# Optimization experiments

Hardware: AMD Instinct MI355X
Metric: run time of the kernel (lower is better)

## Reference

```python
import jax, jax.numpy as jnp
import numpy as np

V, E, H = 50000, 300, 512
L, N, K = 6, 8192, 4


def setup_inputs() -> dict:
    key = jax.random.key(0)
    ks = jax.random.split(key, 12)
    vocab_ix = jax.random.randint(ks[0], (L, N), 0, V)
    child_idx = jax.random.randint(ks[1], (L, N, K), 0, N)
    token_mask = jnp.ones((L, N), dtype=jnp.float32)
    child_mask = (jax.random.uniform(ks[2], (L, N, K)) < 0.75).astype(jnp.float32)
    s = 0.02
    embed = jax.random.normal(ks[3], (V, E), dtype=jnp.float32)
    W_iou = jax.random.normal(ks[4], (E, 3 * H), dtype=jnp.float32) * s
    U_iou = jax.random.normal(ks[5], (H, 3 * H), dtype=jnp.float32) * s
    b_iou = jnp.zeros((3 * H,), dtype=jnp.float32)
    W_f = jax.random.normal(ks[6], (E, H), dtype=jnp.float32) * s
    U_f = jax.random.normal(ks[7], (H, H), dtype=jnp.float32) * s
    b_f = jnp.zeros((H,), dtype=jnp.float32)
    return {"vocab_ix": vocab_ix, "child_idx": child_idx, "token_mask": token_mask,
            "child_mask": child_mask, "embed": embed, "W_iou": W_iou, "U_iou": U_iou,
            "b_iou": b_iou, "W_f": W_f, "U_f": U_f, "b_f": b_f}


def _tree_lstm(vocab_ix, child_idx, token_mask, child_mask,
               embed, W_iou, U_iou, b_iou, W_f, U_f, b_f):
    # bottom-up over levels; level L-1 = leaves (no children -> zero prev states)
    h = jnp.zeros((N, H), dtype=embed.dtype)
    c = jnp.zeros((N, H), dtype=embed.dtype)
    for l in reversed(range(L)):
        # word2vec: embedding lookup; zero vector for non-token nodes
        x = embed[vocab_ix[l]] * token_mask[l][:, None]            # [N, E]
        xWf = x @ W_f                                              # [N, H]
        if l == L - 1:
            h_tilde = jnp.zeros((N, H), dtype=x.dtype)
            fc = jnp.zeros((N, H), dtype=x.dtype)
        else:
            m = child_mask[l][:, :, None]                          # [N, K, 1]
            h_ch = h[child_idx[l]] * m                             # [N, K, H]
            c_ch = c[child_idx[l]] * m                             # [N, K, H]
            h_tilde = h_ch.sum(axis=1)                             # child-sum
            # per-child forget gates (padded slots: c_ch is 0 -> no contribution)
            f = jax.nn.sigmoid(xWf[:, None, :] + jnp.einsum('nkh,hj->nkj', h_ch, U_f) + b_f)
            fc = (f * c_ch).sum(axis=1)
        iou = x @ W_iou + h_tilde @ U_iou + b_iou                  # [N, 3H]
        i, o, u = jnp.split(iou, 3, axis=-1)
        c = jax.nn.sigmoid(i) * jnp.tanh(u) + fc
        h = jax.nn.sigmoid(o) * jnp.tanh(c)
    return h  # outputs[0][1]: hidden states of root level


def reference(vocab_ix, child_idx, token_mask, child_mask,
              embed, W_iou, U_iou, b_iou, W_f, U_f, b_f):
    return _tree_lstm(vocab_ix, child_idx, token_mask, child_mask,
                      embed, W_iou, U_iou, b_iou, W_f, U_f, b_f)
```

## Files before the change

kernel.cpp:

```cpp
#include <hip/hip_runtime.h>
#include <cmath>

#define VSZ  50000
#define EDIM 300
#define EPAD 320
#define HDIM 512
#define LVLS 6
#define NN   8192
#define KCH  4

#define BM 128
#define BN 128
#define BK 32

typedef __attribute__((ext_vector_type(8))) short bf16x8;
typedef __attribute__((ext_vector_type(8))) unsigned short us8;
typedef __attribute__((ext_vector_type(4))) float f32x4;

__device__ __forceinline__ float sigf(float x) { return 1.0f / (1.0f + expf(-x)); }

__device__ __forceinline__ unsigned short f2bf(float f) {
    unsigned u = __float_as_uint(f);
    u += 0x7FFF + ((u >> 16) & 1);
    return (unsigned short)(u >> 16);
}
__device__ __forceinline__ float bf2f(unsigned short h) {
    return __uint_as_float(((unsigned)h) << 16);
}

__device__ __forceinline__ unsigned cvt_pk_bf16(float lo, float hi) {
    unsigned r;
    asm("v_cvt_pk_bf16_f32 %0, %1, %2" : "=v"(r) : "v"(lo), "v"(hi));
    return r;
}

__global__ __launch_bounds__(256) void gconv_k(
    const float* __restrict__ embed, const int* __restrict__ vix,
    const float* __restrict__ tmask, unsigned short* __restrict__ out)
{
    int t  = blockIdx.x * 256 + threadIdx.x;
    int r  = t / (EPAD / 8);
    int j8 = (t - r * (EPAD / 8)) * 8;
    float m = tmask[r];
    int   v = vix[r];
    const float* src = embed + (size_t)v * EDIM + j8;
    us8 o;
    if (j8 + 8 <= EDIM) {
        float4 a = *(const float4*)(src);
        float4 b = *(const float4*)(src + 4);
        const float xs[8] = {a.x, a.y, a.z, a.w, b.x, b.y, b.z, b.w};
#pragma unroll
        for (int j = 0; j < 8; ++j) o[j] = f2bf(xs[j] * m);
    } else {
#pragma unroll
        for (int j = 0; j < 8; ++j) {
            float x = (j8 + j < EDIM) ? src[j] * m : 0.0f;
            o[j] = f2bf(x);
        }
    }
    *(us8*)(out + (size_t)r * EPAD + j8) = o;
}

__global__ __launch_bounds__(256) void wconv_k(
    const float* __restrict__ in, unsigned short* __restrict__ out,
    int Kreal, int Ksp, int Nd)
{
    int t = blockIdx.x * 256 + threadIdx.x;
    int k = t % Ksp;
    int n = t / Ksp;
    out[t] = (k < Kreal) ? f2bf(in[(size_t)k * Nd + n]) : (unsigned short)0;
}

#define GLL(src, dst)                                                        \
    __builtin_amdgcn_global_load_lds(                                        \
        (const __attribute__((address_space(1))) unsigned int*)(src), (dst), 16, 0, 0)

template <int EPI, int NCHUNK>
__global__ __launch_bounds__(256) void mgemm_k(
    const unsigned short* __restrict__ Ab,
    const unsigned short* __restrict__ Bt,
    const float* __restrict__ b_iou, const float* __restrict__ b_f,
    unsigned short* __restrict__ C, int ldc, int Ks)
{
    __shared__ __align__(16) unsigned short smem[6 * BM * BK];

    const int tid  = threadIdx.x;
    const int wave = tid >> 6;
    const int lane = tid & 63;
    const int quad = lane >> 4;
    const int mcol = lane & 15;
    const int wm   = (wave >> 1) * 64;
    const int wn   = (wave & 1) * 64;
    const int band = wave >> 1;

    const int GX   = gridDim.x;
    const int P    = blockIdx.x + GX * blockIdx.y;
    const int g    = P & 7;
    const int s    = P >> 3;
    const int mper = gridDim.y >> 3;
    const int sdiv = s / GX;
    const int my_mt = g * mper + sdiv;
    const int my_ng = s - sdiv * GX;
    const int tile_m = my_mt * BM;

    const int r0  = tid >> 2;
    const int kg0 = (tid & 3) ^ ((r0 >> 1) & 3);
    const int cc1 = tid + 256;
    const int r1  = cc1 >> 2;
    const int kg1 = (cc1 & 3) ^ ((r1 >> 1) & 3);

    const unsigned short* asrc0 = Ab + (size_t)(tile_m + r0) * Ks + kg0 * 8;
    const unsigned short* asrc1 = Ab + (size_t)(tile_m + r1) * Ks + kg1 * 8;

    typedef __attribute__((address_space(3))) unsigned int lds_u32;

    float* eb = reinterpret_cast<float*>(smem);
    const int erl = tid >> 3;
    const int ecg = tid & 7;

#define STAGE3(kk, bo)                                                       \
    {                                                                        \
        GLL(asrc0 + (kk), (lds_u32*)(smem + (bo) + wave * 512));             \
        GLL(asrc1 + (kk), (lds_u32*)(smem + (bo) + 2048 + wave * 512));      \
        GLL(bsrc0 + (kk), (lds_u32*)(smem + (bo) + 4096 + wave * 512));      \
        GLL(bsrc1 + (kk), (lds_u32*)(smem + (bo) + 6144 + wave * 512));      \
    }
#define WAITV4  asm volatile("s_waitcnt vmcnt(4)" ::: "memory")
#define WAITV0  asm volatile("s_waitcnt vmcnt(0)" ::: "memory")
#define BAR     __builtin_amdgcn_s_barrier()

#define COMPUTE(bo)                                                         \
    {                                                                       \
        const unsigned short* AS = smem + (bo);                             \
        const unsigned short* BS = smem + (bo) + 4096;                      \
        bf16x8 afr[4], bfr[4];                                              \
        _Pragma("unroll")                                                   \
        for (int mt = 0; mt < 4; ++mt) {                                    \
            int rw = wm + mt * 16 + mcol;                                   \
            int p  = rw * 4 + (quad ^ ((rw >> 1) & 3));                     \
            afr[mt] = *(const bf16x8*)(AS + p * 8);                         \
        }                                                                   \
        _Pragma("unroll")                                                   \
        for (int nt = 0; nt < 4; ++nt) {                                    \
            int rw = wn + nt * 16 + mcol;                                   \
            int p  = rw * 4 + (quad ^ ((rw >> 1) & 3));                     \
            bfr[nt] = *(const bf16x8*)(BS + p * 8);                         \
        }                                                                   \
        _Pragma("unroll")                                                   \
        for (int mt = 0; mt < 4; ++mt)                                      \
            _Pragma("unroll")                                               \
            for (int nt = 0; nt < 4; ++nt)                                  \
                acc[mt][nt] = __builtin_amdgcn_mfma_f32_16x16x32_bf16(      \
                    afr[mt], bfr[nt], acc[mt][nt], 0, 0, 0);                \
    }

    for (int nc = 0; nc < NCHUNK; ++nc) {
        const int tile_n = (my_ng * NCHUNK + nc) * BN;
        const unsigned short* bsrc0 = Bt + (size_t)(tile_n + r0) * Ks + kg0 * 8;
        const unsigned short* bsrc1 = Bt + (size_t)(tile_n + r1) * Ks + kg1 * 8;

        f32x4 acc[4][4] = {};
        const int nsteps = Ks / BK;

        int bo0 = 0, bo1 = 8192, bo2 = 16384;

        STAGE3(0, bo0);
        STAGE3(BK, bo1);
        WAITV4;
        BAR;

        for (int st = 0; st < nsteps; ++st) {
            const bool pf = (st + 2 < nsteps);
            if (pf) STAGE3((st + 2) * BK, bo2);
            COMPUTE(bo0);
            if (pf) { WAITV4; } else { WAITV0; }
            BAR;
            int t0 = bo0; bo0 = bo1; bo1 = bo2; bo2 = t0;
        }

#pragma unroll
        for (int mt = 0; mt < 4; ++mt) {
            const int rbase = band * 16 + quad * 4;
#pragma unroll
            for (int nt = 0; nt < 4; ++nt) {
                const int cb = wn + nt * 16 + mcol;
                const int gq = cb >> 2;
                const int cl = cb & 3;
#pragma unroll
                for (int rr = 0; rr < 4; ++rr) {
                    const int r = rbase + rr;
                    eb[r * 128 + ((gq ^ (r & 7)) << 2) + cl] = acc[mt][nt][rr];
                }
            }
            __syncthreads();

            const int grow = tile_m + (erl >> 4) * 64 + mt * 16 + (erl & 15);
            const int gcol = tile_n + ecg * 16;
            float v[16];
#pragma unroll
            for (int sxt = 0; sxt < 4; ++sxt) {
                const int pg = (ecg * 4 + sxt) ^ (erl & 7);
                f32x4 q = *(const f32x4*)&eb[erl * 128 + pg * 4];
                v[sxt * 4 + 0] = q[0]; v[sxt * 4 + 1] = q[1];
                v[sxt * 4 + 2] = q[2]; v[sxt * 4 + 3] = q[3];
            }
            if (EPI == 1) {
                const float* bp = (gcol < 3 * HDIM) ? (b_iou + gcol)
                                                    : (b_f + gcol - 3 * HDIM);
                float4 b0 = *(const float4*)(bp);
                float4 b1 = *(const float4*)(bp + 4);
                float4 b2 = *(const float4*)(bp + 8);
                float4 b3 = *(const float4*)(bp + 12);
                const float bb[16] = {b0.x, b0.y, b0.z, b0.w, b1.x, b1.y, b1.z, b1.w,
                                      b2.x, b2.y, b2.z, b2.w, b3.x, b3.y, b3.z, b3.w};
#pragma unroll
                for (int j = 0; j < 16; ++j) v[j] += bb[j];
            }
            unsigned pw[8];
#pragma unroll
            for (int j = 0; j < 8; ++j) pw[j] = cvt_pk_bf16(v[2 * j], v[2 * j + 1]);
            unsigned short* cp = C + (size_t)grow * ldc + gcol;
            *(uint4*)(cp)     = make_uint4(pw[0], pw[1], pw[2], pw[3]);
            *(uint4*)(cp + 8) = make_uint4(pw[4], pw[5], pw[6], pw[7]);
            __syncthreads();
        }
    }
#undef STAGE3
#undef WAITV4
#undef WAITV0
#undef BAR
#undef COMPUTE
}

template <bool LAST>
__global__ __launch_bounds__(256) void gatefc_k(
    const unsigned short* __restrict__ iouxW, const unsigned short* __restrict__ Z,
    const int* __restrict__ cidx, const float* __restrict__ cmask,
    const float* __restrict__ c_prev,
    float* __restrict__ c_new, unsigned short* __restrict__ hb_new,
    float* __restrict__ h_out)
{
    int t  = blockIdx.x * 256 + threadIdx.x;
    int n  = t >> 6;
    int j8 = (t & 63) << 3;
    const unsigned short* xr = iouxW + (size_t)n * 4 * HDIM + j8;
    us8 xi = *(const us8*)xr;
    us8 xo = *(const us8*)(xr + HDIM);
    us8 xu = *(const us8*)(xr + 2 * HDIM);
    us8 xf = *(const us8*)(xr + 3 * HDIM);
    float ia[8], oa[8], ua[8], xw[8], fc[8];
#pragma unroll
    for (int j = 0; j < 8; ++j) {
        ia[j] = bf2f(xi[j]); oa[j] = bf2f(xo[j]);
        ua[j] = bf2f(xu[j]); xw[j] = bf2f(xf[j]);
        fc[j] = 0.0f;
    }
    int4   ci = *(const int4*)&cidx[n * KCH];
    float4 cm = *(const float4*)&cmask[n * KCH];
    const int   cia[4] = {ci.x, ci.y, ci.z, ci.w};
    const float cma[4] = {cm.x, cm.y, cm.z, cm.w};
#pragma unroll
    for (int k = 0; k < KCH; ++k) {
        const float m = cma[k];
        const unsigned short* zr = Z + (size_t)cia[k] * 4 * HDIM + j8;
        us8 zi = *(const us8*)zr;
        us8 zo = *(const us8*)(zr + HDIM);
        us8 zu = *(const us8*)(zr + 2 * HDIM);
        us8 zf = *(const us8*)(zr + 3 * HDIM);
        const float* cpr = c_prev + (size_t)cia[k] * HDIM + j8;
        float4 ca = *(const float4*)cpr;
        float4 cb = *(const float4*)(cpr + 4);
        const float cp[8] = {ca.x, ca.y, ca.z, ca.w, cb.x, cb.y, cb.z, cb.w};
#pragma unroll
        for (int j = 0; j < 8; ++j) {
            ia[j] += m * bf2f(zi[j]);
            oa[j] += m * bf2f(zo[j]);
            ua[j] += m * bf2f(zu[j]);
            fc[j] += sigf(xw[j] + m * bf2f(zf[j])) * m * cp[j];
        }
    }
    float cv[8], hv[8];
#pragma unroll
    for (int j = 0; j < 8; ++j) {
        cv[j] = sigf(ia[j]) * tanhf(ua[j]) + fc[j];
        hv[j] = sigf(oa[j]) * tanhf(cv[j]);
    }
    if (LAST) {
        float4 h0 = make_float4(hv[0], hv[1], hv[2], hv[3]);
        float4 h1 = make_float4(hv[4], hv[5], hv[6], hv[7]);
        *(float4*)(h_out + (size_t)n * HDIM + j8)     = h0;
        *(float4*)(h_out + (size_t)n * HDIM + j8 + 4) = h1;
    } else {
        float4 c0v = make_float4(cv[0], cv[1], cv[2], cv[3]);
        float4 c1v = make_float4(cv[4], cv[5], cv[6], cv[7]);
        *(float4*)(c_new + (size_t)n * HDIM + j8)     = c0v;
        *(float4*)(c_new + (size_t)n * HDIM + j8 + 4) = c1v;
        us8 hb;
#pragma unroll
        for (int j = 0; j < 8; ++j) hb[j] = f2bf(hv[j]);
        *(us8*)(hb_new + (size_t)n * HDIM + j8) = hb;
    }
}

__global__ __launch_bounds__(256) void gateleaf_k(
    const unsigned short* __restrict__ iouxW,
    float* __restrict__ c_new, unsigned short* __restrict__ hb_new)
{
    int t  = blockIdx.x * 256 + threadIdx.x;
    int n  = t >> 6;
    int j8 = (t & 63) << 3;
    const unsigned short* xr = iouxW + (size_t)n * 4 * HDIM + j8;
    us8 xi = *(const us8*)xr;
    us8 xo = *(const us8*)(xr + HDIM);
    us8 xu = *(const us8*)(xr + 2 * HDIM);
    float cv[8], hv[8];
#pragma unroll
    for (int j = 0; j < 8; ++j) {
        cv[j] = sigf(bf2f(xi[j])) * tanhf(bf2f(xu[j]));
        hv[j] = sigf(bf2f(xo[j])) * tanhf(cv[j]);
    }
    float4 c0v = make_float4(cv[0], cv[1], cv[2], cv[3]);
    float4 c1v = make_float4(cv[4], cv[5], cv[6], cv[7]);
    *(float4*)(c_new + (size_t)n * HDIM + j8)     = c0v;
    *(float4*)(c_new + (size_t)n * HDIM + j8 + 4) = c1v;
    us8 hb;
#pragma unroll
    for (int j = 0; j < 8; ++j) hb[j] = f2bf(hv[j]);
    *(us8*)(hb_new + (size_t)n * HDIM + j8) = hb;
}

extern "C" void kernel_launch(void* const* d_in, const int* in_sizes, int n_in,
                              void* d_out, int out_size, void* d_ws, size_t ws_size,
                              hipStream_t stream)
{
    const int*   vocab_ix   = (const int*)d_in[0];
    const int*   child_idx  = (const int*)d_in[1];
    const float* token_mask = (const float*)d_in[2];
    const float* child_mask = (const float*)d_in[3];
    const float* embed      = (const float*)d_in[4];
    const float* W_iou      = (const float*)d_in[5];
    const float* U_iou      = (const float*)d_in[6];
    const float* b_iou      = (const float*)d_in[7];
    const float* W_f        = (const float*)d_in[8];
    const float* U_f        = (const float*)d_in[9];
    const float* b_f        = (const float*)d_in[10];
    float* out = (float*)d_out;

    float* ws = (float*)d_ws;
    float* c0 = ws;
    float* c1 = c0 + (size_t)NN * HDIM;
    unsigned short* usb   = (unsigned short*)(c1 + (size_t)NN * HDIM);
    unsigned short* hb0   = usb;
    unsigned short* hb1   = hb0 + (size_t)NN * HDIM;
    unsigned short* iouxW = hb1 + (size_t)NN * HDIM;
    unsigned short* Z     = iouxW + (size_t)3 * NN * 4 * HDIM;
    unsigned short* AbatA = Z + (size_t)NN * 4 * HDIM;
    unsigned short* AbatB = AbatA + (size_t)3 * NN * EPAD;
    unsigned short* WtALL = AbatB + (size_t)3 * NN * EPAD;
    unsigned short* UtALL = WtALL + (size_t)4 * HDIM * EPAD;

    dim3 blk(256);

    const int grows = 3 * NN * (EPAD / 8) / 256;
    gconv_k<<<dim3(grows), blk, 0, stream>>>(embed, vocab_ix + (size_t)3 * NN,
                                             token_mask + (size_t)3 * NN, AbatA);
    gconv_k<<<dim3(grows), blk, 0, stream>>>(embed, vocab_ix, token_mask, AbatB);
    wconv_k<<<dim3(3 * HDIM * EPAD / 256), blk, 0, stream>>>(W_iou, WtALL, EDIM, EPAD, 3 * HDIM);
    wconv_k<<<dim3(HDIM * EPAD / 256),     blk, 0, stream>>>(W_f, WtALL + (size_t)3 * HDIM * EPAD, EDIM, EPAD, HDIM);
    wconv_k<<<dim3(3 * HDIM * HDIM / 256), blk, 0, stream>>>(U_iou, UtALL, HDIM, HDIM, 3 * HDIM);
    wconv_k<<<dim3(HDIM * HDIM / 256),     blk, 0, stream>>>(U_f, UtALL + (size_t)3 * HDIM * HDIM, HDIM, HDIM, HDIM);

    unsigned short* bbuf[2] = { hb0, hb1 };
    float*          cbuf[2] = { c0,  c1  };

    const int ew_blocks = NN * HDIM / 8 / 256;

    mgemm_k<1, 2><<<dim3(8, 3 * NN / BM), blk, 0, stream>>>(
        AbatA, WtALL, b_iou, b_f, iouxW, 4 * HDIM, EPAD);

    for (int l = LVLS - 1; l >= 0; --l) {
        const int p = (LVLS - 1 - l);
        unsigned short* hb_new  = bbuf[p & 1];
        float*          c_new   = cbuf[p & 1];
        unsigned short* hb_prev = bbuf[(p & 1) ^ 1];
        float*          c_prev  = cbuf[(p & 1) ^ 1];
        const int*   cix = child_idx  + (size_t)l * NN * KCH;
        const float* cm  = child_mask + (size_t)l * NN * KCH;
        const unsigned short* ix_l =
            iouxW + (size_t)((l >= 3) ? (l - 3) : l) * NN * 4 * HDIM;

        if (l == LVLS - 1) {
            gateleaf_k<<<dim3(ew_blocks), blk, 0, stream>>>(ix_l, c_new, hb_new);
        } else {
            mgemm_k<0, 2><<<dim3(8, NN / BM), blk, 0, stream>>>(
                hb_prev, UtALL, nullptr, nullptr, Z, 4 * HDIM, HDIM);

            if (l == 0) {
                gatefc_k<true><<<dim3(ew_blocks), blk, 0, stream>>>(
                    ix_l, Z, cix, cm, c_prev, nullptr, nullptr, out);
            } else {
                gatefc_k<false><<<dim3(ew_blocks), blk, 0, stream>>>(
                    ix_l, Z, cix, cm, c_prev, c_new, hb_new, nullptr);
            }
        }

        if (l == 3) {
            mgemm_k<1, 2><<<dim3(8, 3 * NN / BM), blk, 0, stream>>>(
                AbatB, WtALL, b_iou, b_f, iouxW, 4 * HDIM, EPAD);
        }
    }
}
```

Measured before the change: 598.5 us.

## Swap MFMA operands for direct bf16 epilogue stores; split recurrent GEMM grid

```diff
diff --git a/kernel.cpp b/kernel.cpp
--- a/kernel.cpp
+++ b/kernel.cpp
@@ -91,7 +91,6 @@
     const int mcol = lane & 15;
     const int wm   = (wave >> 1) * 64;
     const int wn   = (wave & 1) * 64;
-    const int band = wave >> 1;
 
     const int GX   = gridDim.x;
     const int P    = blockIdx.x + GX * blockIdx.y;
@@ -113,10 +112,6 @@
     const unsigned short* asrc1 = Ab + (size_t)(tile_m + r1) * Ks + kg1 * 8;
 
     typedef __attribute__((address_space(3))) unsigned int lds_u32;
-
-    float* eb = reinterpret_cast<float*>(smem);
-    const int erl = tid >> 3;
-    const int ecg = tid & 7;
 
 #define STAGE3(kk, bo)                                                       \
     {                                                                        \
@@ -151,7 +146,7 @@
             _Pragma("unroll")                                               \
             for (int nt = 0; nt < 4; ++nt)                                  \
                 acc[mt][nt] = __builtin_amdgcn_mfma_f32_16x16x32_bf16(      \
-                    afr[mt], bfr[nt], acc[mt][nt], 0, 0, 0);                \
+                    bfr[nt], afr[mt], acc[mt][nt], 0, 0, 0);                \
     }
 
     for (int nc = 0; nc < NCHUNK; ++nc) {
@@ -180,50 +175,25 @@
 
 #pragma unroll
         for (int mt = 0; mt < 4; ++mt) {
-            const int rbase = band * 16 + quad * 4;
+            const int grow = tile_m + wm + mt * 16 + mcol;
+            unsigned short* crow = C + (size_t)grow * ldc;
 #pragma unroll
             for (int nt = 0; nt < 4; ++nt) {
-                const int cb = wn + nt * 16 + mcol;
-                const int gq = cb >> 2;
-                const int cl = cb & 3;
-#pragma unroll
-                for (int rr = 0; rr < 4; ++rr) {
-                    const int r = rbase + rr;
-                    eb[r * 128 + ((gq ^ (r & 7)) << 2) + cl] = acc[mt][nt][rr];
+                const int col0 = tile_n + wn + nt * 16 + quad * 4;
+                float v0 = acc[mt][nt][0], v1 = acc[mt][nt][1];
+                float v2 = acc[mt][nt][2], v3 = acc[mt][nt][3];
+                if (EPI == 1) {
+                    const float* bp = (col0 < 3 * HDIM) ? (b_iou + col0)
+                                                        : (b_f + col0 - 3 * HDIM);
+                    float4 bb = *(const float4*)bp;
+                    v0 += bb.x; v1 += bb.y; v2 += bb.z; v3 += bb.w;
                 }
+                unsigned p0 = cvt_pk_bf16(v0, v1);
+                unsigned p1 = cvt_pk_bf16(v2, v3);
+                *(uint2*)(crow + col0) = make_uint2(p0, p1);
             }
-            __syncthreads();
-
-            const int grow = tile_m + (erl >> 4) * 64 + mt * 16 + (erl & 15);
-            const int gcol = tile_n + ecg * 16;
-            float v[16];
-#pragma unroll
-            for (int sxt = 0; sxt < 4; ++sxt) {
-                const int pg = (ecg * 4 + sxt) ^ (erl & 7);
-                f32x4 q = *(const f32x4*)&eb[erl * 128 + pg * 4];
-                v[sxt * 4 + 0] = q[0]; v[sxt * 4 + 1] = q[1];
-                v[sxt * 4 + 2] = q[2]; v[sxt * 4 + 3] = q[3];
-            }
-            if (EPI == 1) {
-                const float* bp = (gcol < 3 * HDIM) ? (b_iou + gcol)
-                                                    : (b_f + gcol - 3 * HDIM);
-                float4 b0 = *(const float4*)(bp);
-                float4 b1 = *(const float4*)(bp + 4);
-                float4 b2 = *(const float4*)(bp + 8);
-                float4 b3 = *(const float4*)(bp + 12);
-                const float bb[16] = {b0.x, b0.y, b0.z, b0.w, b1.x, b1.y, b1.z, b1.w,
-                                      b2.x, b2.y, b2.z, b2.w, b3.x, b3.y, b3.z, b3.w};
-#pragma unroll
-                for (int j = 0; j < 16; ++j) v[j] += bb[j];
-            }
-            unsigned pw[8];
-#pragma unroll
-            for (int j = 0; j < 8; ++j) pw[j] = cvt_pk_bf16(v[2 * j], v[2 * j + 1]);
-            unsigned short* cp = C + (size_t)grow * ldc + gcol;
-            *(uint4*)(cp)     = make_uint4(pw[0], pw[1], pw[2], pw[3]);
-            *(uint4*)(cp + 8) = make_uint4(pw[4], pw[5], pw[6], pw[7]);
-            __syncthreads();
-        }
+        }
+        if (nc + 1 < NCHUNK) BAR;
     }
 #undef STAGE3
 #undef WAITV4
@@ -392,7 +362,7 @@
         if (l == LVLS - 1) {
             gateleaf_k<<<dim3(ew_blocks), blk, 0, stream>>>(ix_l, c_new, hb_new);
         } else {
-            mgemm_k<0, 2><<<dim3(8, NN / BM), blk, 0, stream>>>(
+            mgemm_k<0, 1><<<dim3(16, NN / BM), blk, 0, stream>>>(
                 hb_prev, UtALL, nullptr, nullptr, Z, 4 * HDIM, HDIM);
 
             if (l == 0) {
```

Measured after the change: 623.0 us. +4.1%, slower.
